# Kernel optimization log

Measured on AMD Instinct MI355X. Metric: run time of the kernel, lower is better.

Reference implementation:

```python
import jax, jax.numpy as jnp
import numpy as np

jax.config.update("jax_enable_x64", True)  # torch casts to double for matrix_exp

EPS_DIAG = 1e-6


def setup_inputs() -> dict:
    key = jax.random.key(0)
    B, D, NB, S = 32, 128, 8, 128
    ks = jax.random.split(key, 9)
    return {
        "z0r": jax.random.normal(ks[0], (B, D), jnp.float32),
        "z0i": jax.random.normal(ks[1], (B, D), jnp.float32),
        # uniform grid: dt = time_steps[0] = 0.01, diffs == dt (uniform branch)
        "time_steps": (jnp.arange(S, dtype=jnp.float32) + 1.0) * 0.01,
        "k_coeffs": jax.random.normal(ks[2], (B, NB), jnp.float32),
        "r_coeffs": jax.random.normal(ks[3], (B, NB), jnp.float32),
        "alpha": jax.random.normal(ks[4], (B, 1), jnp.float32),
        "beta": jax.random.normal(ks[5], (B, 1), jnp.float32),
        "K_bases": jax.random.normal(ks[6], (NB, D, D), jnp.float32) * 0.01,
        "R_bases": jax.random.normal(ks[7], (NB, D, D), jnp.float32) * 0.01,
    }


def _build_generator(k_coeffs, r_coeffs, alpha, beta, K_bases, R_bases):
    # A = alpha * skew(K_sum) + beta * -(R_sum^T @ R_sum), per batch element
    K_sum = jnp.einsum("bn,nij->bij", k_coeffs, K_bases)
    R_sum = jnp.einsum("bn,nij->bij", r_coeffs, R_bases)
    skew = K_sum - jnp.swapaxes(K_sum, -1, -2)
    neg_gram = -jnp.einsum("bji,bjk->bik", R_sum, R_sum)  # -(R^T @ R)
    return alpha[..., None] * skew + beta[..., None] * neg_gram  # (B, D, D)


def _propagators(A, time_steps, uniform):
    D = A.shape[-1]
    S = time_steps.shape[0]
    if uniform:
        dt = time_steps[0]
        A64 = A.astype(jnp.float64) * dt.astype(jnp.float64) + EPS_DIAG * jnp.eye(D, dtype=jnp.float64)
        M = jax.vmap(jax.scipy.linalg.expm)(A64).astype(jnp.complex64)  # (B, D, D)
        # cumulative matrix powers M, M^2, ..., M^S via O(log S) associative scan
        Ms = jnp.broadcast_to(M[:, None], (M.shape[0], S, D, D))
        props = jax.lax.associative_scan(jnp.matmul, Ms, axis=1)
    else:
        A_t = A[:, None].astype(jnp.float64) * time_steps.astype(jnp.float64)[None, :, None, None]
        props = jax.vmap(jax.vmap(jax.scipy.linalg.expm))(A_t).astype(jnp.complex64)
    return props  # (B, S, D, D)


def reference(z0r, z0i, time_steps, k_coeffs, r_coeffs, alpha, beta, K_bases, R_bases):
    ts = np.asarray(time_steps)
    uniform = ts.shape[0] <= 1 or np.allclose(ts[1:] - ts[:-1], ts[0], atol=1e-6)
    A = _build_generator(k_coeffs, r_coeffs, alpha, beta, K_bases, R_bases)
    props = _propagators(A, time_steps, uniform)
    z = (z0r + 1j * z0i).astype(jnp.complex64)  # (B, D)
    # z_evolved[b, s, o] = sum_i z[b, i] * props[b, s, o, i]
    return jnp.einsum("bi,bsoi->bso", z, props)
```

## Files before the change

### kernel.cpp

```cpp
#include <hip/hip_runtime.h>

#define BATCH   32
#define DIM     128
#define NBASES  8
#define SSTEPS  128
#define LDA     136

typedef __attribute__((ext_vector_type(8))) short s8v;
typedef __attribute__((ext_vector_type(4))) short s4v;
typedef __attribute__((ext_vector_type(4))) float f4v;

__device__ __forceinline__ f4v mf(s8v a, s8v b, f4v c) {
    return __builtin_amdgcn_mfma_f32_16x16x32_bf16(a, b, c, 0, 0, 0);
}
__device__ __forceinline__ s8v ld8(const short* p) {
    return *reinterpret_cast<const s8v*>(p);
}
__device__ __forceinline__ s4v ld4(const short* p) {
    return *reinterpret_cast<const s4v*>(p);
}
__device__ __forceinline__ void st4(short* p, s4v v) {
    *reinterpret_cast<s4v*>(p) = v;
}
__device__ __forceinline__ float upbf(short h) {
    return __uint_as_float(((unsigned)(unsigned short)h) << 16);
}
__device__ __forceinline__ void splitbf(float v, short& hi, short& lo) {
    const unsigned u = __float_as_uint(v);
    hi = (short)(u >> 16);
    const float fh = __uint_as_float(u & 0xffff0000u);
    lo = (short)(__float_as_uint(v - fh) >> 16);
}

__device__ __forceinline__ void write_out(float* __restrict__ outF, int b, int sidx,
                                          int o, int c, float val,
                                          int interleaved, int out_size)
{
    if (interleaved) {
        const int oi = ((b * SSTEPS + sidx) * DIM + o) * 2 + c;
        if (oi < out_size) outF[oi] = val;
    } else if (c == 0) {
        const int oi = (b * SSTEPS + sidx) * DIM + o;
        if (oi < out_size) outF[oi] = val;
    }
}

template<bool TRO, bool NMO>
__device__ __forceinline__ void mm_full(const short* __restrict__ Ah,
                                        const short* __restrict__ Al,
                                        const short* __restrict__ Bh,
                                        const short* __restrict__ Bl,
                                        f4v acc[2][2], f4v acct[2][2],
                                        int mb, int nb, int lane)
{
    const int l15 = lane & 15, quad = lane >> 4;
    #pragma unroll
    for (int kk = 0; kk < DIM; kk += 32) {
        const int ko = kk + quad * 8;
        s8v ah[2], al[2], bh[2], bl[2];
        #pragma unroll
        for (int i = 0; i < 2; ++i) {
            ah[i] = ld8(Ah + (mb + i * 16 + l15) * LDA + ko);
            al[i] = ld8(Al + (mb + i * 16 + l15) * LDA + ko);
            bh[i] = ld8(Bh + (nb + i * 16 + l15) * LDA + ko);
            bl[i] = ld8(Bl + (nb + i * 16 + l15) * LDA + ko);
        }
        #pragma unroll
        for (int mi = 0; mi < 2; ++mi)
            #pragma unroll
            for (int ni = 0; ni < 2; ++ni) {
                if (TRO) {
                    acc[mi][ni] = mf(ah[mi], bh[ni], acc[mi][ni]);
                    acc[mi][ni] = mf(ah[mi], bl[ni], acc[mi][ni]);
                    acc[mi][ni] = mf(al[mi], bh[ni], acc[mi][ni]);
                }
                if (NMO) {
                    acct[ni][mi] = mf(bh[ni], ah[mi], acct[ni][mi]);
                    acct[ni][mi] = mf(bl[ni], ah[mi], acct[ni][mi]);
                    acct[ni][mi] = mf(bh[ni], al[mi], acct[ni][mi]);
                }
            }
    }
}

__global__ __launch_bounds__(1024) __attribute__((amdgpu_waves_per_eu(4, 4)))
void htg_mfma(const float* __restrict__ z0r, const float* __restrict__ z0i,
              const float* __restrict__ ts,  const float* __restrict__ kco,
              const float* __restrict__ rco, const float* __restrict__ alp,
              const float* __restrict__ bet, const float* __restrict__ KB,
              const float* __restrict__ RB,  float* __restrict__ outF,
              int interleaved, int out_size)
{
    __shared__ short nm_hi[DIM * LDA], nm_lo[DIM * LDA];
    __shared__ short tr_hi[DIM * LDA], tr_lo[DIM * LDA];
    __shared__ short ht_hi[32 * LDA],  ht_lo[32 * LDA];

    const int b = blockIdx.x, t = threadIdx.x;
    const int w = t >> 6, lane = t & 63;
    const int l15 = lane & 15, quad = lane >> 4;
    const f4v z4 = {0.f, 0.f, 0.f, 0.f};
    const int mb = (w & 3) * 32, nb = (w >> 2) * 32;

    {
        float rc[NBASES], kc[NBASES];
        #pragma unroll
        for (int n = 0; n < NBASES; ++n) {
            rc[n] = rco[b * NBASES + n];
            kc[n] = kco[b * NBASES + n];
        }
        #pragma unroll
        for (int q = 0; q < 4; ++q) {
            const int e = q * 4096 + t * 4;
            float4 r4 = {0.f, 0.f, 0.f, 0.f}, k4 = {0.f, 0.f, 0.f, 0.f};
            #pragma unroll
            for (int n = 0; n < NBASES; ++n) {
                const float4 rv = *reinterpret_cast<const float4*>(RB + n * DIM * DIM + e);
                const float4 kv = *reinterpret_cast<const float4*>(KB + n * DIM * DIM + e);
                r4.x += rc[n] * rv.x; r4.y += rc[n] * rv.y;
                r4.z += rc[n] * rv.z; r4.w += rc[n] * rv.w;
                k4.x += kc[n] * kv.x; k4.y += kc[n] * kv.y;
                k4.z += kc[n] * kv.z; k4.w += kc[n] * kv.w;
            }
            const int r = e >> 7, c = e & 127;
            const float rr[4] = {r4.x, r4.y, r4.z, r4.w};
            const float kk[4] = {k4.x, k4.y, k4.z, k4.w};
            s4v kh, kl;
            #pragma unroll
            for (int j = 0; j < 4; ++j) {
                short hi, lo;
                splitbf(rr[j], hi, lo);
                tr_hi[(c + j) * LDA + r] = hi; tr_lo[(c + j) * LDA + r] = lo;
                splitbf(kk[j], hi, lo);
                kh[j] = hi; kl[j] = lo;
            }
            st4(&nm_hi[r * LDA + c], kh);
            st4(&nm_lo[r * LDA + c], kl);
        }
        if (t < 2 * DIM) {
            const int c = t >> 7, o = t & 127;
            const float zv = (c == 0) ? z0r[b * DIM + o] : z0i[b * DIM + o];
            short hi, lo; splitbf(zv, hi, lo);
            ht_hi[c * LDA + o] = hi; ht_lo[c * LDA + o] = lo;
        }
    }
    __syncthreads();

    f4v acc[2][2], acct[2][2];
    float xsave[2][2][4];

    float kd[2][2][4], kdT[2][2][4];
    #pragma unroll
    for (int mi = 0; mi < 2; ++mi)
        #pragma unroll
        for (int ni = 0; ni < 2; ++ni) {
            {
                const int row0 = mb + mi * 16 + quad * 4;
                const int col  = nb + ni * 16 + l15;
                const s4v k2h = ld4(&nm_hi[col * LDA + row0]);
                const s4v k2l = ld4(&nm_lo[col * LDA + row0]);
                #pragma unroll
                for (int r = 0; r < 4; ++r)
                    kd[mi][ni][r] = (upbf(nm_hi[(row0 + r) * LDA + col]) +
                                     upbf(nm_lo[(row0 + r) * LDA + col]))
                                  - (upbf(k2h[r]) + upbf(k2l[r]));
            }
            {
                const int rt0 = nb + mi * 16 + quad * 4;
                const int ct  = mb + ni * 16 + l15;
                const s4v k1h = ld4(&nm_hi[ct * LDA + rt0]);
                const s4v k1l = ld4(&nm_lo[ct * LDA + rt0]);
                #pragma unroll
                for (int r = 0; r < 4; ++r)
                    kdT[mi][ni][r] = (upbf(k1h[r]) + upbf(k1l[r]))
                                   - (upbf(nm_hi[(rt0 + r) * LDA + ct]) +
                                      upbf(nm_lo[(rt0 + r) * LDA + ct]));
            }
        }
    #pragma unroll
    for (int i = 0; i < 2; ++i)
        #pragma unroll
        for (int j = 0; j < 2; ++j) { acc[i][j] = z4; acct[i][j] = z4; }
    mm_full<true, true>(tr_hi, tr_lo, tr_hi, tr_lo, acc, acct, mb, nb, lane);
    __syncthreads();
    {
        const float alpha = alp[b], beta = bet[b], dtf = ts[0];
        #pragma unroll
        for (int mi = 0; mi < 2; ++mi)
            #pragma unroll
            for (int ni = 0; ni < 2; ++ni) {
                const int row0 = mb + mi * 16 + quad * 4;
                const int col  = nb + ni * 16 + l15;
                s4v h4, l4;
                #pragma unroll
                for (int r = 0; r < 4; ++r) {
                    float x = (alpha * kd[mi][ni][r] - beta * acc[mi][ni][r]) * dtf;
                    if (row0 + r == col) x += 1e-6f;
                    xsave[mi][ni][r] = x;
                    short hi, lo;
                    splitbf(x, hi, lo);
                    h4[r] = hi; l4[r] = lo;
                }
                st4(&tr_hi[col * LDA + row0], h4);
                st4(&tr_lo[col * LDA + row0], l4);
            }
        #pragma unroll
        for (int ti = 0; ti < 2; ++ti)
            #pragma unroll
            for (int tj = 0; tj < 2; ++tj) {
                const int rt0 = nb + ti * 16 + quad * 4;
                const int ct  = mb + tj * 16 + l15;
                s4v h4, l4;
                #pragma unroll
                for (int r = 0; r < 4; ++r) {
                    float x = (alpha * kdT[ti][tj][r] - beta * acct[ti][tj][r]) * dtf;
                    if (ct == rt0 + r) x += 1e-6f;
                    short hi, lo;
                    splitbf(x, hi, lo);
                    h4[r] = hi; l4[r] = lo;
                }
                st4(&nm_hi[ct * LDA + rt0], h4);
                st4(&nm_lo[ct * LDA + rt0], l4);
            }
    }
    __syncthreads();

    #pragma unroll
    for (int i = 0; i < 2; ++i)
        #pragma unroll
        for (int j = 0; j < 2; ++j) { acc[i][j] = z4; acct[i][j] = z4; }
    mm_full<true, true>(nm_hi, nm_lo, tr_hi, tr_lo, acc, acct, mb, nb, lane);
    __syncthreads();
    #pragma unroll
    for (int mi = 0; mi < 2; ++mi)
        #pragma unroll
        for (int ni = 0; ni < 2; ++ni) {
            const int row0 = mb + mi * 16 + quad * 4;
            const int col  = nb + ni * 16 + l15;
            s4v h4, l4;
            #pragma unroll
            for (int r = 0; r < 4; ++r) {
                const int row = row0 + r;
                const float xv = xsave[mi][ni][r];
                const float cv = acc[mi][ni][r];
                const float a2 = xv * (1.f / 6.f) + cv * (1.f / 24.f);
                xsave[mi][ni][r] = ((row == col) ? 1.f : 0.f) + xv + 0.5f * cv;
                short hi, lo;
                splitbf(a2, hi, lo);
                h4[r] = hi; l4[r] = lo;
            }
            st4(&tr_hi[col * LDA + row0], h4);
            st4(&tr_lo[col * LDA + row0], l4);
        }
    #pragma unroll
    for (int ti = 0; ti < 2; ++ti)
        #pragma unroll
        for (int tj = 0; tj < 2; ++tj) {
            const int rt0 = nb + ti * 16 + quad * 4;
            const int ct  = mb + tj * 16 + l15;
            s4v h4, l4;
            #pragma unroll
            for (int r = 0; r < 4; ++r) {
                short hi, lo;
                splitbf(acct[ti][tj][r], hi, lo);
                h4[r] = hi; l4[r] = lo;
            }
            st4(&nm_hi[ct * LDA + rt0], h4);
            st4(&nm_lo[ct * LDA + rt0], l4);
        }
    __syncthreads();

    #pragma unroll
    for (int mi = 0; mi < 2; ++mi)
        #pragma unroll
        for (int ni = 0; ni < 2; ++ni)
            #pragma unroll
            for (int r = 0; r < 4; ++r) acc[mi][ni][r] = xsave[mi][ni][r];
    mm_full<true, false>(nm_hi, nm_lo, tr_hi, tr_lo, acc, acct, mb, nb, lane);
    __syncthreads();
    #pragma unroll
    for (int mi = 0; mi < 2; ++mi)
        #pragma unroll
        for (int ni = 0; ni < 2; ++ni) {
            const int row0 = mb + mi * 16 + quad * 4;
            const int col  = nb + ni * 16 + l15;
            s4v h4, l4;
            #pragma unroll
            for (int r = 0; r < 4; ++r) {
                short hi, lo;
                splitbf(acc[mi][ni][r], hi, lo);
                nm_hi[(row0 + r) * LDA + col] = hi;
                nm_lo[(row0 + r) * LDA + col] = lo;
                h4[r] = hi; l4[r] = lo;
            }
            st4(&tr_hi[col * LDA + row0], h4);
            st4(&tr_lo[col * LDA + row0], l4);
        }
    __syncthreads();

    #pragma unroll
    for (int stage = 0; stage < 3; ++stage) {
        const int J = 1 << stage;
        f4v ar = z4;
        #pragma unroll
        for (int i = 0; i < 2; ++i)
            #pragma unroll
            for (int j = 0; j < 2; ++j) { acc[i][j] = z4; acct[i][j] = z4; }
        if (w < 8) {
            #pragma unroll
            for (int kk = 0; kk < DIM; kk += 32) {
                const int ko = kk + quad * 8;
                const s8v rah = ld8(nm_hi + (w * 16 + l15) * LDA + ko);
                const s8v ral = ld8(nm_lo + (w * 16 + l15) * LDA + ko);
                const s8v rbh = ld8(ht_hi + l15 * LDA + ko);
                const s8v rbl = ld8(ht_lo + l15 * LDA + ko);
                ar = mf(rah, rbh, ar);
                ar = mf(rah, rbl, ar);
                ar = mf(ral, rbh, ar);
            }
        }
        mm_full<true, true>(nm_hi, nm_lo, tr_hi, tr_lo, acc, acct, mb, nb, lane);
        __syncthreads();
        if (w < 8 && l15 < 2 * J) {
            const int o0 = w * 16 + quad * 4;
            const int sidx = (l15 >> 1) + J - 1;
            s4v h4, l4;
            #pragma unroll
            for (int r = 0; r < 4; ++r) {
                short hi, lo;
                splitbf(ar[r], hi, lo);
                h4[r] = hi; l4[r] = lo;
                write_out(outF, b, sidx, o0 + r, l15 & 1, ar[r], interleaved, out_size);
            }
            st4(&ht_hi[(l15 + 2 * J) * LDA + o0], h4);
            st4(&ht_lo[(l15 + 2 * J) * LDA + o0], l4);
        }
        #pragma unroll
        for (int mi = 0; mi < 2; ++mi)
            #pragma unroll
            for (int ni = 0; ni < 2; ++ni) {
                const int row0 = mb + mi * 16 + quad * 4;
                const int col  = nb + ni * 16 + l15;
                s4v h4, l4;
                #pragma unroll
                for (int r = 0; r < 4; ++r) {
                    short hi, lo;
                    splitbf(acc[mi][ni][r], hi, lo);
                    h4[r] = hi; l4[r] = lo;
                }
                st4(&tr_hi[col * LDA + row0], h4);
                st4(&tr_lo[col * LDA + row0], l4);
            }
        #pragma unroll
        for (int ti = 0; ti < 2; ++ti)
            #pragma unroll
            for (int tj = 0; tj < 2; ++tj) {
                const int rt0 = nb + ti * 16 + quad * 4;
                const int ct  = mb + tj * 16 + l15;
                s4v h4, l4;
                #pragma unroll
                for (int r = 0; r < 4; ++r) {
                    short hi, lo;
                    splitbf(acct[ti][tj][r], hi, lo);
                    h4[r] = hi; l4[r] = lo;
                }
                st4(&nm_hi[ct * LDA + rt0], h4);
                st4(&nm_lo[ct * LDA + rt0], l4);
            }
        __syncthreads();
    }

    {
        const int J = 8;
        f4v ar = z4;
        #pragma unroll
        for (int i = 0; i < 2; ++i)
            #pragma unroll
            for (int j = 0; j < 2; ++j) acct[i][j] = z4;
        if (w < 8) {
            #pragma unroll
            for (int kk = 0; kk < DIM; kk += 32) {
                const int ko = kk + quad * 8;
                const s8v rah = ld8(nm_hi + (w * 16 + l15) * LDA + ko);
                const s8v ral = ld8(nm_lo + (w * 16 + l15) * LDA + ko);
                const s8v rbh = ld8(ht_hi + l15 * LDA + ko);
                const s8v rbl = ld8(ht_lo + l15 * LDA + ko);
                ar = mf(rah, rbh, ar);
                ar = mf(rah, rbl, ar);
                ar = mf(ral, rbh, ar);
            }
        }
        mm_full<false, true>(nm_hi, nm_lo, tr_hi, tr_lo, acc, acct, mb, nb, lane);
        __syncthreads();
        if (w < 8 && l15 < 2 * J) {
            const int o0 = w * 16 + quad * 4;
            const int sidx = (l15 >> 1) + J - 1;
            s4v h4, l4;
            #pragma unroll
            for (int r = 0; r < 4; ++r) {
                short hi, lo;
                splitbf(ar[r], hi, lo);
                h4[r] = hi; l4[r] = lo;
                write_out(outF, b, sidx, o0 + r, l15 & 1, ar[r], interleaved, out_size);
            }
            st4(&ht_hi[(l15 + 2 * J) * LDA + o0], h4);
            st4(&ht_lo[(l15 + 2 * J) * LDA + o0], l4);
        }
        #pragma unroll
        for (int ti = 0; ti < 2; ++ti)
            #pragma unroll
            for (int tj = 0; tj < 2; ++tj) {
                const int rt0 = nb + ti * 16 + quad * 4;
                const int ct  = mb + tj * 16 + l15;
                s4v h4, l4;
                #pragma unroll
                for (int r = 0; r < 4; ++r) {
                    short hi, lo;
                    splitbf(acct[ti][tj][r], hi, lo);
                    h4[r] = hi; l4[r] = lo;
                }
                st4(&nm_hi[ct * LDA + rt0], h4);
                st4(&nm_lo[ct * LDA + rt0], l4);
            }
        __syncthreads();
    }

    const int sw = w >> 1, ct = w & 1;
    s8v vah[4], val[4];
    #pragma unroll
    for (int k4 = 0; k4 < 4; ++k4) {
        const int ko = k4 * 32 + quad * 8;
        vah[k4] = ld8(nm_hi + (sw * 16 + l15) * LDA + ko);
        val[k4] = ld8(nm_lo + (sw * 16 + l15) * LDA + ko);
    }
    short *rh_hi = ht_hi, *rh_lo = ht_lo;
    short *wh_hi = tr_hi, *wh_lo = tr_lo;
    #pragma unroll
    for (int q = 1; q <= 8; ++q) {
        f4v a2 = z4;
        #pragma unroll
        for (int k4 = 0; k4 < 4; ++k4) {
            const int ko = k4 * 32 + quad * 8;
            const s8v bh = ld8(rh_hi + (ct * 16 + l15) * LDA + ko);
            const s8v bl = ld8(rh_lo + (ct * 16 + l15) * LDA + ko);
            a2 = mf(vah[k4], bh, a2);
            a2 = mf(vah[k4], bl, a2);
            a2 = mf(val[k4], bh, a2);
        }
        {
            const int o0 = sw * 16 + quad * 4;
            const int n = ct * 16 + l15;
            const int sidx = 16 * q + (n >> 1) - 1;
            s4v h4, l4;
            #pragma unroll
            for (int r = 0; r < 4; ++r) {
                short hi, lo;
                splitbf(a2[r], hi, lo);
                h4[r] = hi; l4[r] = lo;
                if (sidx < SSTEPS)
                    write_out(outF, b, sidx, o0 + r, n & 1, a2[r], interleaved, out_size);
            }
            if (q < 8) {
                st4(&wh_hi[n * LDA + o0], h4);
                st4(&wh_lo[n * LDA + o0], l4);
            }
        }
        __syncthreads();
        short* tp;
        tp = rh_hi; rh_hi = wh_hi; wh_hi = tp;
        tp = rh_lo; rh_lo = wh_lo; wh_lo = tp;
    }
}

extern "C" void kernel_launch(void* const* d_in, const int* in_sizes, int n_in,
                              void* d_out, int out_size, void* d_ws, size_t ws_size,
                              hipStream_t stream)
{
    (void)in_sizes; (void)n_in; (void)d_ws; (void)ws_size;
    const float* z0r = (const float*)d_in[0];
    const float* z0i = (const float*)d_in[1];
    const float* ts  = (const float*)d_in[2];
    const float* kco = (const float*)d_in[3];
    const float* rco = (const float*)d_in[4];
    const float* alp = (const float*)d_in[5];
    const float* bet = (const float*)d_in[6];
    const float* KB  = (const float*)d_in[7];
    const float* RB  = (const float*)d_in[8];
    float* outF = (float*)d_out;

    const int interleaved = (out_size >= 2 * BATCH * SSTEPS * DIM) ? 1 : 0;

    htg_mfma<<<dim3(BATCH), dim3(1024), 0, stream>>>(
        z0r, z0i, ts, kco, rco, alp, bet, KB, RB, outF, interleaved, out_size);
}
```

Before: 118.4 us.

## Split basis-coefficient summation into a separate wide prekernel using workspace

Adds a separate kernel that computes the per-batch K and R basis sums across 256 blocks and writes them to the workspace. The main kernel then loads these precomputed sums instead of reading all 8 basis matrices per block. The goal is to spread the memory-bound summation over many more CUs than the 32 blocks of the main kernel. The cost is an extra launch and a round trip through global memory. The old path is kept as a fallback when no workspace is available.

New measurement: 121.3 us. 2.5% more time.

```diff
diff --git a/kernel.cpp b/kernel.cpp
--- a/kernel.cpp
+++ b/kernel.cpp
@@ -83,13 +83,48 @@
     }
 }
 
+__global__ __launch_bounds__(256)
+void sum_kr(const float* __restrict__ kco, const float* __restrict__ rco,
+            const float* __restrict__ KB,  const float* __restrict__ RB,
+            float* __restrict__ ws)
+{
+    const int b = blockIdx.x >> 3, s = blockIdx.x & 7, t = threadIdx.x;
+    const int boff = s * 16 * DIM + t * 8;
+    float kc[NBASES], rc[NBASES];
+    #pragma unroll
+    for (int n = 0; n < NBASES; ++n) {
+        kc[n] = kco[b * NBASES + n];
+        rc[n] = rco[b * NBASES + n];
+    }
+    float4 ka = {0.f,0.f,0.f,0.f}, kb4 = {0.f,0.f,0.f,0.f};
+    float4 ra = {0.f,0.f,0.f,0.f}, rb4 = {0.f,0.f,0.f,0.f};
+    #pragma unroll
+    for (int n = 0; n < NBASES; ++n) {
+        const float4 k0 = *reinterpret_cast<const float4*>(KB + n * DIM * DIM + boff);
+        const float4 k1 = *reinterpret_cast<const float4*>(KB + n * DIM * DIM + boff + 4);
+        const float4 r0 = *reinterpret_cast<const float4*>(RB + n * DIM * DIM + boff);
+        const float4 r1 = *reinterpret_cast<const float4*>(RB + n * DIM * DIM + boff + 4);
+        ka.x += kc[n] * k0.x; ka.y += kc[n] * k0.y; ka.z += kc[n] * k0.z; ka.w += kc[n] * k0.w;
+        kb4.x += kc[n] * k1.x; kb4.y += kc[n] * k1.y; kb4.z += kc[n] * k1.z; kb4.w += kc[n] * k1.w;
+        ra.x += rc[n] * r0.x; ra.y += rc[n] * r0.y; ra.z += rc[n] * r0.z; ra.w += rc[n] * r0.w;
+        rb4.x += rc[n] * r1.x; rb4.y += rc[n] * r1.y; rb4.z += rc[n] * r1.z; rb4.w += rc[n] * r1.w;
+    }
+    float* Ks = ws;
+    float* Rs = ws + BATCH * DIM * DIM;
+    *reinterpret_cast<float4*>(Ks + b * DIM * DIM + boff)     = ka;
+    *reinterpret_cast<float4*>(Ks + b * DIM * DIM + boff + 4) = kb4;
+    *reinterpret_cast<float4*>(Rs + b * DIM * DIM + boff)     = ra;
+    *reinterpret_cast<float4*>(Rs + b * DIM * DIM + boff + 4) = rb4;
+}
+
+template<int PRE>
 __global__ __launch_bounds__(1024) __attribute__((amdgpu_waves_per_eu(4, 4)))
 void htg_mfma(const float* __restrict__ z0r, const float* __restrict__ z0i,
               const float* __restrict__ ts,  const float* __restrict__ kco,
               const float* __restrict__ rco, const float* __restrict__ alp,
               const float* __restrict__ bet, const float* __restrict__ KB,
-              const float* __restrict__ RB,  float* __restrict__ outF,
-              int interleaved, int out_size)
+              const float* __restrict__ RB,  const float* __restrict__ wsum,
+              float* __restrict__ outF, int interleaved, int out_size)
 {
     __shared__ short nm_hi[DIM * LDA], nm_lo[DIM * LDA];
     __shared__ short tr_hi[DIM * LDA], tr_lo[DIM * LDA];
@@ -101,7 +136,36 @@
     const f4v z4 = {0.f, 0.f, 0.f, 0.f};
     const int mb = (w & 3) * 32, nb = (w >> 2) * 32;
 
-    {
+    if (PRE) {
+        const float* Ks = wsum + b * DIM * DIM;
+        const float* Rs = wsum + BATCH * DIM * DIM + b * DIM * DIM;
+        #pragma unroll
+        for (int q = 0; q < 4; ++q) {
+            const int e = q * 4096 + t * 4;
+            const float4 k4 = *reinterpret_cast<const float4*>(Ks + e);
+            const float4 r4 = *reinterpret_cast<const float4*>(Rs + e);
+            const int r = e >> 7, c = e & 127;
+            const float rr[4] = {r4.x, r4.y, r4.z, r4.w};
+            const float kk[4] = {k4.x, k4.y, k4.z, k4.w};
+            s4v kh, kl;
+            #pragma unroll
+            for (int j = 0; j < 4; ++j) {
+                short hi, lo;
+                splitbf(rr[j], hi, lo);
+                tr_hi[(c + j) * LDA + r] = hi; tr_lo[(c + j) * LDA + r] = lo;
+                splitbf(kk[j], hi, lo);
+                kh[j] = hi; kl[j] = lo;
+            }
+            st4(&nm_hi[r * LDA + c], kh);
+            st4(&nm_lo[r * LDA + c], kl);
+        }
+        if (t < 2 * DIM) {
+            const int c = t >> 7, o = t & 127;
+            const float zv = (c == 0) ? z0r[b * DIM + o] : z0i[b * DIM + o];
+            short hi, lo; splitbf(zv, hi, lo);
+            ht_hi[c * LDA + o] = hi; ht_lo[c * LDA + o] = lo;
+        }
+    } else {
         float rc[NBASES], kc[NBASES];
         #pragma unroll
         for (int n = 0; n < NBASES; ++n) {
@@ -475,7 +539,7 @@
                               void* d_out, int out_size, void* d_ws, size_t ws_size,
                               hipStream_t stream)
 {
-    (void)in_sizes; (void)n_in; (void)d_ws; (void)ws_size;
+    (void)in_sizes; (void)n_in;
     const float* z0r = (const float*)d_in[0];
     const float* z0i = (const float*)d_in[1];
     const float* ts  = (const float*)d_in[2];
@@ -488,7 +552,15 @@
     float* outF = (float*)d_out;
 
     const int interleaved = (out_size >= 2 * BATCH * SSTEPS * DIM) ? 1 : 0;
-
-    htg_mfma<<<dim3(BATCH), dim3(1024), 0, stream>>>(
-        z0r, z0i, ts, kco, rco, alp, bet, KB, RB, outF, interleaved, out_size);
-}
+    const size_t ws_needed = (size_t)2 * BATCH * DIM * DIM * sizeof(float);
+
+    if (d_ws != nullptr && ws_size >= ws_needed) {
+        float* ws = (float*)d_ws;
+        sum_kr<<<dim3(BATCH * 8), dim3(256), 0, stream>>>(kco, rco, KB, RB, ws);
+        htg_mfma<1><<<dim3(BATCH), dim3(1024), 0, stream>>>(
+            z0r, z0i, ts, kco, rco, alp, bet, KB, RB, ws, outF, interleaved, out_size);
+    } else {
+        htg_mfma<0><<<dim3(BATCH), dim3(1024), 0, stream>>>(
+            z0r, z0i, ts, kco, rco, alp, bet, KB, RB, nullptr, outF, interleaved, out_size);
+    }
+}
```
